# Performance work log

Measured on AMD Instinct MI355X. Metric: run time of the kernel, lower is better.

## Reference

```python
import jax, jax.numpy as jnp
import numpy as np

SCALE_FLOOR = 0.001
N_SOURCES = 16


def setup_inputs() -> dict:
    key = jax.random.key(0)
    ks = jax.random.split(key, 8)
    n, d_in, d = 131072, 1024, 512
    x = jax.random.normal(ks[0], (n, d_in), dtype=jnp.float32)
    source_ids = jax.random.randint(ks[1], (n,), 0, N_SOURCES, dtype=jnp.int64)
    # backbone: single Linear(d_in -> d)
    Wb = jax.random.normal(ks[2], (d_in, d), dtype=jnp.float32) / np.sqrt(d_in)
    bb = jax.random.normal(ks[3], (d,), dtype=jnp.float32) * 0.01
    # pooled head: Linear(d -> 2)
    Wp = jax.random.normal(ks[4], (d, 2), dtype=jnp.float32) / np.sqrt(d)
    bp = jax.random.normal(ks[5], (2,), dtype=jnp.float32) * 0.01
    # per-source heads stacked: [S, d, 2], [S, 2]
    Ws = jax.random.normal(ks[6], (N_SOURCES, d, 2), dtype=jnp.float32) / np.sqrt(d)
    bs = jax.random.normal(ks[7], (N_SOURCES, 2), dtype=jnp.float32) * 0.01
    return {"x": x, "source_ids": source_ids, "Wb": Wb, "bb": bb,
            "Wp": Wp, "bp": bp, "Ws": Ws, "bs": bs}


def _head(raw):
    # raw: (n, 2) -> (mu, scale) with softplus + floor on scale
    mu = raw[:, 0]
    scale = jax.nn.softplus(raw[:, 1]) + SCALE_FLOOR
    return mu, scale


def reference(x, source_ids, Wb, bb, Wp, bp, Ws, bs):
    # backbone embedding: (n, d)
    emb = x @ Wb + bb
    # pooled head
    pooled_mu, pooled_scale = _head(emb @ Wp + bp)
    # routed per-source heads: compute all tiny heads, then gather per row.
    # raw_all: (n, S, 2); S*2 is tiny so this beats gather of per-row weights.
    raw_all = jnp.einsum('nd,sdk->nsk', emb, Ws) + bs[None, :, :]
    raw_sel = jnp.take_along_axis(raw_all, source_ids[:, None, None], axis=1)[:, 0, :]
    src_mu, src_scale = _head(raw_sel)
    # all source ids fall in [0, N_SOURCES), so every row is covered
    # (matches the torch loop where unmatched rows would stay zero).
    return emb, pooled_mu, pooled_scale, src_mu, src_scale
```

## Files before the change

### kernel.cpp

```cpp
#include <hip/hip_runtime.h>

typedef short bf16x8 __attribute__((ext_vector_type(8)));
typedef float f32x4 __attribute__((ext_vector_type(4)));

#define NROWS 131072L
#define DIN 1024
#define DEMB 512
#define NEXT 640

__device__ __forceinline__ unsigned short f2bf(float f) {
  unsigned u = __float_as_uint(f);
  u += 0x7FFFu + ((u >> 16) & 1u);
  return (unsigned short)(u >> 16);
}

__device__ __forceinline__ unsigned pkhi(float a, float b) {
  unsigned ua = __float_as_uint(a) + 0x8000u;
  unsigned ub = __float_as_uint(b) + 0x8000u;
  return __builtin_amdgcn_perm(ub, ua, 0x07060302u);
}

__device__ __forceinline__ float softplusf(float v) {
  return fmaxf(v, 0.f) + log1pf(expf(-fabsf(v)));
}

__global__ __launch_bounds__(256) void wb_transpose(const float* __restrict__ Wb,
                                                    unsigned short* __restrict__ WbT) {
  int g = blockIdx.x * 256 + threadIdx.x;
  int n = g & 511;
  int kb = g >> 9;
  unsigned short tmp[8];
#pragma unroll
  for (int j = 0; j < 8; ++j)
    tmp[j] = f2bf(Wb[(kb * 8 + j) * DEMB + n]);
  uint4 v;
  v.x = (unsigned)tmp[0] | ((unsigned)tmp[1] << 16);
  v.y = (unsigned)tmp[2] | ((unsigned)tmp[3] << 16);
  v.z = (unsigned)tmp[4] | ((unsigned)tmp[5] << 16);
  v.w = (unsigned)tmp[6] | ((unsigned)tmp[7] << 16);
  *(uint4*)(WbT + (long)n * DIN + kb * 8) = v;
}

__global__ void zero_tail(unsigned* __restrict__ p) {
  p[blockIdx.x * 256 + threadIdx.x] = 0u;
}

__global__ __launch_bounds__(256) void wfold_rows(const float* __restrict__ Wb,
                                                  const float* __restrict__ Wp,
                                                  const float* __restrict__ Ws,
                                                  unsigned short* __restrict__ WbT) {
  int w = threadIdx.x >> 6, lane = threadIdx.x & 63;
  int k = blockIdx.x * 4 + w;
  if (lane >= 34) return;
  const float* src;
  if (lane < 2) src = Wp + lane;
  else { int s = (lane - 2) >> 1; src = Ws + s * 1024 + (lane & 1); }
  const float* wrow = Wb + (long)k * DEMB;
  float acc = 0.f;
#pragma unroll 8
  for (int d = 0; d < DEMB; ++d) acc = fmaf(wrow[d], src[2 * d], acc);
  WbT[(long)(512 + lane) * DIN + k] = f2bf(acc);
}

__global__ void bfold_k(const float* __restrict__ bb, const float* __restrict__ Wp,
                        const float* __restrict__ bp, const float* __restrict__ Ws,
                        const float* __restrict__ bs, float* __restrict__ bf) {
  int j = threadIdx.x;
  if (j >= 34) return;
  const float* src; float bias;
  if (j < 2) { src = Wp + j; bias = bp[j]; }
  else { int s = (j - 2) >> 1; src = Ws + s * 1024 + (j & 1); bias = bs[s * 2 + (j & 1)]; }
  float acc = bias;
  for (int d = 0; d < DEMB; ++d) acc = fmaf(bb[d], src[2 * d], acc);
  bf[j] = acc;
}

#define SB __builtin_amdgcn_sched_barrier(0)

__global__ __launch_bounds__(256, 2) void gemm_fused(
    const float* __restrict__ x, const unsigned short* __restrict__ wbt,
    const float* __restrict__ bb, const int* __restrict__ sid,
    const float* __restrict__ bfold, float* __restrict__ out) {
  __shared__ __align__(16) char SM[65536];
  char* const As0 = SM;
  char* const As1 = SM + 16384;
  char* const Bs0 = SM + 32768;
  char* const Bs1 = SM + 49152;

  const int t = threadIdx.x;
  const int lane = t & 63;
  const int wid = t >> 6;
  const int wm = wid >> 1, wn = wid & 1;

  const int bid = blockIdx.x;
  const int swz = (bid & 7) * 640 + (bid >> 3);
  const int mtile = swz / 5;
  const int ntile = swz - mtile * 5;
  const long m0 = (long)mtile * 128;
  const int n0 = ntile * 128;

  const int arow = t >> 4;
  const int acol8 = (t & 15) * 8;
  const int abyte = arow * 128 + (acol8 ^ ((arow & 7) << 4));
  const float* xbase = x + (m0 + arow) * DIN + (t & 15) * 4;

  const int bn = wid * 32 + (lane >> 3);
  const int bg = (lane & 7) ^ (lane >> 3);
  const unsigned short* bsrc = wbt + (long)(n0 + bn) * DIN + bg * 8;

  const int l15 = lane & 15, lg = lane >> 4;
  const int s3 = lane & 7;
  const int kg0 = ((lg ^ s3) << 4);
  const int ardrow = (wm * 64 + l15) * 128;
  const int brdrow = (wn * 64 + l15) * 128;

  f32x4 acc[4][4] = {};
  float4 aA[8], aB[8];

  auto loadA = [&](float4* d, int k0) {
#pragma unroll
    for (int p = 0; p < 8; ++p)
      d[p] = *(const float4*)(xbase + (long)p * 16 * DIN + k0);
  };
  auto stageB = [&](char* Bw, int k0) {
#pragma unroll
    for (int i = 0; i < 4; ++i) {
      const unsigned short* gp = bsrc + (long)i * 8 * DIN + k0;
      __builtin_amdgcn_global_load_lds(
          (const __attribute__((address_space(1))) void*)gp,
          (__attribute__((address_space(3))) void*)(Bw + wid * 4096 + i * 1024),
          16, 0, 0);
    }
  };
  auto writeA = [&](char* Aw, const float4* d) {
#pragma unroll
    for (int p = 0; p < 8; ++p) {
      uint2 v;
      v.x = pkhi(d[p].x, d[p].y);
      v.y = pkhi(d[p].z, d[p].w);
      *(uint2*)(Aw + abyte + p * 2048) = v;
    }
  };
  auto compute = [&](const char* Ac, const char* Bc) {
#pragma unroll
    for (int ks = 0; ks < 2; ++ks) {
      const int kgo = kg0 ^ (ks << 6);
      bf16x8 af[4], bfv[4];
#pragma unroll
      for (int i = 0; i < 4; ++i) {
        af[i]  = *(const bf16x8*)(Ac + ardrow + i * 2048 + kgo);
        bfv[i] = *(const bf16x8*)(Bc + brdrow + i * 2048 + kgo);
      }
      __builtin_amdgcn_s_setprio(1);
#pragma unroll
      for (int mi = 0; mi < 4; ++mi)
#pragma unroll
        for (int ni = 0; ni < 4; ++ni)
          acc[mi][ni] = __builtin_amdgcn_mfma_f32_16x16x32_bf16(af[mi], bfv[ni],
                                                               acc[mi][ni], 0, 0, 0);
      __builtin_amdgcn_s_setprio(0);
    }
  };

  loadA(aA, 0);
  stageB(Bs0, 0);
  SB; asm volatile("s_waitcnt vmcnt(4)" ::: "memory"); SB;
  writeA(As0, aA);
  loadA(aB, 64);
  SB; asm volatile("s_waitcnt vmcnt(8) lgkmcnt(0)" ::: "memory"); SB;
  __builtin_amdgcn_s_barrier();

#pragma unroll 1
  for (int tb = 0; tb < 14; tb += 2) {
    stageB(Bs1, (tb + 1) * 64);
    loadA(aA, (tb + 2) * 64);
    compute(As0, Bs0);
    SB; asm volatile("s_waitcnt vmcnt(12)" ::: "memory"); SB;
    writeA(As1, aB);
    SB; asm volatile("s_waitcnt vmcnt(8) lgkmcnt(0)" ::: "memory"); SB;
    __builtin_amdgcn_s_barrier();
    stageB(Bs0, (tb + 2) * 64);
    loadA(aB, (tb + 3) * 64);
    compute(As1, Bs1);
    SB; asm volatile("s_waitcnt vmcnt(12)" ::: "memory"); SB;
    writeA(As0, aA);
    SB; asm volatile("s_waitcnt vmcnt(8) lgkmcnt(0)" ::: "memory"); SB;
    __builtin_amdgcn_s_barrier();
  }

  stageB(Bs1, 15 * 64);
  compute(As0, Bs0);
  SB; asm volatile("s_waitcnt vmcnt(4)" ::: "memory"); SB;
  writeA(As1, aB);
  SB; asm volatile("s_waitcnt vmcnt(0) lgkmcnt(0)" ::: "memory"); SB;
  __builtin_amdgcn_s_barrier();
  compute(As1, Bs1);

  if (ntile < 4) {
    const int colg = n0 + wn * 64 + l15;
    float bbv[4];
#pragma unroll
    for (int ni = 0; ni < 4; ++ni) bbv[ni] = bb[colg + ni * 16];
#pragma unroll
    for (int mi = 0; mi < 4; ++mi) {
      const long rbase = m0 + wm * 64 + mi * 16 + lg * 4;
#pragma unroll
      for (int ni = 0; ni < 4; ++ni)
#pragma unroll
        for (int r = 0; r < 4; ++r)
          out[(rbase + r) * DEMB + colg + ni * 16] = acc[mi][ni][r] + bbv[ni];
    }
  } else {
    __syncthreads();
    float* hl = (float*)SM;
    if (wn == 0) {
#pragma unroll
      for (int ni = 0; ni < 3; ++ni) {
#pragma unroll
        for (int mi = 0; mi < 4; ++mi)
#pragma unroll
          for (int r = 0; r < 4; ++r) {
            int row = wm * 64 + mi * 16 + lg * 4 + r;
            int col = l15 + ni * 16;
            if (col < 35) hl[row * 35 + col] = acc[mi][ni][r];
          }
      }
    }
    __syncthreads();
    if (t < 128) {
      const long row = m0 + t;
      const int s = sid[row];
      const float v0 = hl[t * 35 + 0] + bfold[0];
      const float v1 = hl[t * 35 + 1] + bfold[1];
      const float v2 = hl[t * 35 + 2 + 2 * s] + bfold[2 + 2 * s];
      const float v3 = hl[t * 35 + 3 + 2 * s] + bfold[3 + 2 * s];
      float* hp = out + NROWS * DEMB;
      hp[row] = v0;
      hp[NROWS + row] = softplusf(v1) + 0.001f;
      hp[2 * NROWS + row] = v2;
      hp[3 * NROWS + row] = softplusf(v3) + 0.001f;
    }
  }
}

extern "C" void kernel_launch(void* const* d_in, const int* in_sizes, int n_in,
                              void* d_out, int out_size, void* d_ws, size_t ws_size,
                              hipStream_t stream) {
  const float* x  = (const float*)d_in[0];
  const int* sid  = (const int*)d_in[1];
  const float* Wb = (const float*)d_in[2];
  const float* bb = (const float*)d_in[3];
  const float* Wp = (const float*)d_in[4];
  const float* bp = (const float*)d_in[5];
  const float* Ws = (const float*)d_in[6];
  const float* bs = (const float*)d_in[7];
  float* out = (float*)d_out;
  unsigned short* WbT = (unsigned short*)d_ws;
  float* bfoldp = (float*)(WbT + (long)NEXT * DIN);

  wb_transpose<<<256, 256, 0, stream>>>(Wb, WbT);
  zero_tail<<<188, 256, 0, stream>>>((unsigned*)(WbT + 546 * DIN));
  wfold_rows<<<256, 256, 0, stream>>>(Wb, Wp, Ws, WbT);
  bfold_k<<<1, 64, 0, stream>>>(bb, Wp, bp, Ws, bs, bfoldp);
  gemm_fused<<<5120, 256, 0, stream>>>(x, WbT, bb, sid, bfoldp, out);
}
```

Measured before the change: 341.7 us.

## Enlarge GEMM tile to 256x256 with 8 waves and interleaved load/MFMA schedule

Changes the fused GEMM from 128x128 tiles with 4 waves to 256x256 tiles with 8 waves per block, using 128KB of LDS and one block per CU. The extended N dimension is padded to 768, so the head columns now occupy a full 256-wide tile. A new per-K-tile schedule interleaves global loads, LDS reads and MFMA groups with barriers. The larger tile raises operand reuse and cuts redundant x reads, but it pads more wasted compute into the head tile, lowers occupancy and adds more barriers.

```diff
diff --git a/kernel.cpp b/kernel.cpp
--- a/kernel.cpp
+++ b/kernel.cpp
@@ -6,7 +6,7 @@
 #define NROWS 131072L
 #define DIN 1024
 #define DEMB 512
-#define NEXT 640
+#define NEXT 768
 
 __device__ __forceinline__ unsigned short f2bf(float f) {
   unsigned u = __float_as_uint(f);
@@ -77,133 +77,162 @@
 
 #define SB __builtin_amdgcn_sched_barrier(0)
 
-__global__ __launch_bounds__(256, 2) void gemm_fused(
+__global__ __launch_bounds__(512, 1) void gemm_fused(
     const float* __restrict__ x, const unsigned short* __restrict__ wbt,
     const float* __restrict__ bb, const int* __restrict__ sid,
     const float* __restrict__ bfold, float* __restrict__ out) {
-  __shared__ __align__(16) char SM[65536];
+  __shared__ __align__(16) char SM[131072];
   char* const As0 = SM;
-  char* const As1 = SM + 16384;
-  char* const Bs0 = SM + 32768;
-  char* const Bs1 = SM + 49152;
+  char* const As1 = SM + 32768;
+  char* const Bs0 = SM + 65536;
+  char* const Bs1 = SM + 98304;
 
   const int t = threadIdx.x;
   const int lane = t & 63;
   const int wid = t >> 6;
-  const int wm = wid >> 1, wn = wid & 1;
+  const int wm = wid >> 2, wn = wid & 3;
 
   const int bid = blockIdx.x;
-  const int swz = (bid & 7) * 640 + (bid >> 3);
-  const int mtile = swz / 5;
-  const int ntile = swz - mtile * 5;
-  const long m0 = (long)mtile * 128;
-  const int n0 = ntile * 128;
+  const int swz = (bid & 7) * 192 + (bid >> 3);
+  const int mtile = swz / 3;
+  const int ntile = swz - mtile * 3;
+  const long m0 = (long)mtile * 256;
+  const int n0 = ntile * 256;
 
   const int arow = t >> 4;
-  const int acol8 = (t & 15) * 8;
-  const int abyte = arow * 128 + (acol8 ^ ((arow & 7) << 4));
+  const int abyte = arow * 128 + (((t & 15) * 8) ^ ((arow & 7) << 4));
   const float* xbase = x + (m0 + arow) * DIN + (t & 15) * 4;
 
-  const int bn = wid * 32 + (lane >> 3);
-  const int bg = (lane & 7) ^ (lane >> 3);
-  const unsigned short* bsrc = wbt + (long)(n0 + bn) * DIN + bg * 8;
+  const int bsg = (t & 7) ^ ((t >> 3) & 7);
+  const unsigned short* bsrc = wbt + (long)(n0 + (t >> 3)) * DIN + bsg * 8;
 
   const int l15 = lane & 15, lg = lane >> 4;
-  const int s3 = lane & 7;
-  const int kg0 = ((lg ^ s3) << 4);
-  const int ardrow = (wm * 64 + l15) * 128;
-  const int brdrow = (wn * 64 + l15) * 128;
-
-  f32x4 acc[4][4] = {};
-  float4 aA[8], aB[8];
-
-  auto loadA = [&](float4* d, int k0) {
-#pragma unroll
-    for (int p = 0; p < 8; ++p)
-      d[p] = *(const float4*)(xbase + (long)p * 16 * DIN + k0);
-  };
-  auto stageB = [&](char* Bw, int k0) {
-#pragma unroll
-    for (int i = 0; i < 4; ++i) {
-      const unsigned short* gp = bsrc + (long)i * 8 * DIN + k0;
+  const int kg0 = ((lg ^ (l15 & 7)) << 4);
+  const int aBase = (wm * 128 + l15) * 128;
+  const int bBase = (wn * 64 + l15) * 128;
+
+  f32x4 acc[8][4] = {};
+  bf16x8 afc[8];
+  float4 areg[8];
+
+  auto loadA4 = [&](int pbase, int k0) {
+#pragma unroll
+    for (int p = 0; p < 4; ++p)
+      areg[pbase + p] = *(const float4*)(xbase + (long)(pbase + p) * 32 * DIN + k0);
+  };
+  auto gloadB2 = [&](char* Bw, int ibase, int k0) {
+#pragma unroll
+    for (int i = 0; i < 2; ++i) {
+      const unsigned short* gp = bsrc + (long)(ibase + i) * 64 * DIN + k0;
       __builtin_amdgcn_global_load_lds(
           (const __attribute__((address_space(1))) void*)gp,
-          (__attribute__((address_space(3))) void*)(Bw + wid * 4096 + i * 1024),
+          (__attribute__((address_space(3))) void*)(Bw + (ibase + i) * 8192 + t * 16),
           16, 0, 0);
     }
   };
-  auto writeA = [&](char* Aw, const float4* d) {
+  auto writeA = [&](char* Aw) {
 #pragma unroll
     for (int p = 0; p < 8; ++p) {
       uint2 v;
-      v.x = pkhi(d[p].x, d[p].y);
-      v.y = pkhi(d[p].z, d[p].w);
-      *(uint2*)(Aw + abyte + p * 2048) = v;
-    }
-  };
-  auto compute = [&](const char* Ac, const char* Bc) {
-#pragma unroll
-    for (int ks = 0; ks < 2; ++ks) {
-      const int kgo = kg0 ^ (ks << 6);
-      bf16x8 af[4], bfv[4];
-#pragma unroll
-      for (int i = 0; i < 4; ++i) {
-        af[i]  = *(const bf16x8*)(Ac + ardrow + i * 2048 + kgo);
-        bfv[i] = *(const bf16x8*)(Bc + brdrow + i * 2048 + kgo);
-      }
-      __builtin_amdgcn_s_setprio(1);
-#pragma unroll
-      for (int mi = 0; mi < 4; ++mi)
-#pragma unroll
-        for (int ni = 0; ni < 4; ++ni)
-          acc[mi][ni] = __builtin_amdgcn_mfma_f32_16x16x32_bf16(af[mi], bfv[ni],
-                                                               acc[mi][ni], 0, 0, 0);
-      __builtin_amdgcn_s_setprio(0);
-    }
-  };
-
-  loadA(aA, 0);
-  stageB(Bs0, 0);
+      v.x = pkhi(areg[p].x, areg[p].y);
+      v.y = pkhi(areg[p].z, areg[p].w);
+      *(uint2*)(Aw + abyte + p * 4096) = v;
+    }
+  };
+  auto readA8 = [&](const char* Ac, int ks) {
+    const int ko = kg0 ^ (ks << 6);
+#pragma unroll
+    for (int mi = 0; mi < 8; ++mi)
+      afc[mi] = *(const bf16x8*)(Ac + aBase + mi * 2048 + ko);
+  };
+  auto mfma16 = [&](bf16x8 b0, bf16x8 b1, int ni) {
+    __builtin_amdgcn_s_setprio(1);
+#pragma unroll
+    for (int mi = 0; mi < 8; ++mi)
+      acc[mi][ni] = __builtin_amdgcn_mfma_f32_16x16x32_bf16(afc[mi], b0, acc[mi][ni], 0, 0, 0);
+#pragma unroll
+    for (int mi = 0; mi < 8; ++mi)
+      acc[mi][ni + 1] = __builtin_amdgcn_mfma_f32_16x16x32_bf16(afc[mi], b1, acc[mi][ni + 1], 0, 0, 0);
+    __builtin_amdgcn_s_setprio(0);
+  };
+  auto bread = [&](const char* Bc, int ni, int ks) {
+    return *(const bf16x8*)(Bc + bBase + ni * 2048 + (kg0 ^ (ks << 6)));
+  };
+
+  auto tileS = [&](const char* Ac, const char* Bc, char* Aw, char* Bw, int kS) {
+    bf16x8 b0, b1;
+    readA8(Ac, 0); b0 = bread(Bc, 0, 0); b1 = bread(Bc, 1, 0);
+    loadA4(0, kS); gloadB2(Bw, 0, kS);
+    __builtin_amdgcn_s_barrier();
+    SB; asm volatile("s_waitcnt lgkmcnt(0)" ::: "memory"); SB;
+    mfma16(b0, b1, 0);
+    __builtin_amdgcn_s_barrier();
+    b0 = bread(Bc, 2, 0); b1 = bread(Bc, 3, 0);
+    loadA4(4, kS); gloadB2(Bw, 2, kS);
+    __builtin_amdgcn_s_barrier();
+    SB; asm volatile("s_waitcnt lgkmcnt(0)" ::: "memory"); SB;
+    mfma16(b0, b1, 2);
+    __builtin_amdgcn_s_barrier();
+    readA8(Ac, 1); b0 = bread(Bc, 0, 1); b1 = bread(Bc, 1, 1);
+    __builtin_amdgcn_s_barrier();
+    SB; asm volatile("s_waitcnt lgkmcnt(0)" ::: "memory"); SB;
+    mfma16(b0, b1, 0);
+    __builtin_amdgcn_s_barrier();
+    b0 = bread(Bc, 2, 1); b1 = bread(Bc, 3, 1);
+    SB; asm volatile("s_waitcnt vmcnt(2)" ::: "memory"); SB;
+    writeA(Aw);
+    __builtin_amdgcn_s_barrier();
+    SB; asm volatile("s_waitcnt lgkmcnt(0)" ::: "memory"); SB;
+    mfma16(b0, b1, 2);
+    SB; asm volatile("s_waitcnt vmcnt(0) lgkmcnt(0)" ::: "memory"); SB;
+    __builtin_amdgcn_s_barrier();
+  };
+  auto tileN = [&](const char* Ac, const char* Bc) {
+    bf16x8 b0, b1;
+    readA8(Ac, 0); b0 = bread(Bc, 0, 0); b1 = bread(Bc, 1, 0);
+    __builtin_amdgcn_s_barrier();
+    SB; asm volatile("s_waitcnt lgkmcnt(0)" ::: "memory"); SB;
+    mfma16(b0, b1, 0);
+    __builtin_amdgcn_s_barrier();
+    b0 = bread(Bc, 2, 0); b1 = bread(Bc, 3, 0);
+    __builtin_amdgcn_s_barrier();
+    SB; asm volatile("s_waitcnt lgkmcnt(0)" ::: "memory"); SB;
+    mfma16(b0, b1, 2);
+    __builtin_amdgcn_s_barrier();
+    readA8(Ac, 1); b0 = bread(Bc, 0, 1); b1 = bread(Bc, 1, 1);
+    __builtin_amdgcn_s_barrier();
+    SB; asm volatile("s_waitcnt lgkmcnt(0)" ::: "memory"); SB;
+    mfma16(b0, b1, 0);
+    __builtin_amdgcn_s_barrier();
+    b0 = bread(Bc, 2, 1); b1 = bread(Bc, 3, 1);
+    __builtin_amdgcn_s_barrier();
+    SB; asm volatile("s_waitcnt lgkmcnt(0)" ::: "memory"); SB;
+    mfma16(b0, b1, 2);
+  };
+
+  loadA4(0, 0); loadA4(4, 0);
+  gloadB2(Bs0, 0, 0); gloadB2(Bs0, 2, 0);
   SB; asm volatile("s_waitcnt vmcnt(4)" ::: "memory"); SB;
-  writeA(As0, aA);
-  loadA(aB, 64);
-  SB; asm volatile("s_waitcnt vmcnt(8) lgkmcnt(0)" ::: "memory"); SB;
+  writeA(As0);
+  SB; asm volatile("s_waitcnt vmcnt(0) lgkmcnt(0)" ::: "memory"); SB;
   __builtin_amdgcn_s_barrier();
 
 #pragma unroll 1
   for (int tb = 0; tb < 14; tb += 2) {
-    stageB(Bs1, (tb + 1) * 64);
-    loadA(aA, (tb + 2) * 64);
-    compute(As0, Bs0);
-    SB; asm volatile("s_waitcnt vmcnt(12)" ::: "memory"); SB;
-    writeA(As1, aB);
-    SB; asm volatile("s_waitcnt vmcnt(8) lgkmcnt(0)" ::: "memory"); SB;
-    __builtin_amdgcn_s_barrier();
-    stageB(Bs0, (tb + 2) * 64);
-    loadA(aB, (tb + 3) * 64);
-    compute(As1, Bs1);
-    SB; asm volatile("s_waitcnt vmcnt(12)" ::: "memory"); SB;
-    writeA(As0, aA);
-    SB; asm volatile("s_waitcnt vmcnt(8) lgkmcnt(0)" ::: "memory"); SB;
-    __builtin_amdgcn_s_barrier();
+    tileS(As0, Bs0, As1, Bs1, (tb + 1) * 64);
+    tileS(As1, Bs1, As0, Bs0, (tb + 2) * 64);
   }
-
-  stageB(Bs1, 15 * 64);
-  compute(As0, Bs0);
-  SB; asm volatile("s_waitcnt vmcnt(4)" ::: "memory"); SB;
-  writeA(As1, aB);
-  SB; asm volatile("s_waitcnt vmcnt(0) lgkmcnt(0)" ::: "memory"); SB;
-  __builtin_amdgcn_s_barrier();
-  compute(As1, Bs1);
-
-  if (ntile < 4) {
+  tileS(As0, Bs0, As1, Bs1, 15 * 64);
+  tileN(As1, Bs1);
+
+  if (ntile < 2) {
     const int colg = n0 + wn * 64 + l15;
     float bbv[4];
 #pragma unroll
     for (int ni = 0; ni < 4; ++ni) bbv[ni] = bb[colg + ni * 16];
 #pragma unroll
-    for (int mi = 0; mi < 4; ++mi) {
-      const long rbase = m0 + wm * 64 + mi * 16 + lg * 4;
+    for (int mi = 0; mi < 8; ++mi) {
+      const long rbase = m0 + wm * 128 + mi * 16 + lg * 4;
 #pragma unroll
       for (int ni = 0; ni < 4; ++ni)
 #pragma unroll
@@ -217,17 +246,17 @@
 #pragma unroll
       for (int ni = 0; ni < 3; ++ni) {
 #pragma unroll
-        for (int mi = 0; mi < 4; ++mi)
+        for (int mi = 0; mi < 8; ++mi)
 #pragma unroll
           for (int r = 0; r < 4; ++r) {
-            int row = wm * 64 + mi * 16 + lg * 4 + r;
-            int col = l15 + ni * 16;
+            int row = wm * 128 + mi * 16 + lg * 4 + r;
+            int col = ni * 16 + l15;
             if (col < 35) hl[row * 35 + col] = acc[mi][ni][r];
           }
       }
     }
     __syncthreads();
-    if (t < 128) {
+    if (t < 256) {
       const long row = m0 + t;
       const int s = sid[row];
       const float v0 = hl[t * 35 + 0] + bfold[0];
@@ -259,8 +288,8 @@
   float* bfoldp = (float*)(WbT + (long)NEXT * DIN);
 
   wb_transpose<<<256, 256, 0, stream>>>(Wb, WbT);
-  zero_tail<<<188, 256, 0, stream>>>((unsigned*)(WbT + 546 * DIN));
+  zero_tail<<<444, 256, 0, stream>>>((unsigned*)(WbT + 546 * DIN));
   wfold_rows<<<256, 256, 0, stream>>>(Wb, Wp, Ws, WbT);
   bfold_k<<<1, 64, 0, stream>>>(bb, Wp, bp, Ws, bs, bfoldp);
-  gemm_fused<<<5120, 256, 0, stream>>>(x, WbT, bb, sid, bfoldp, out);
-}
+  gemm_fused<<<1536, 512, 0, stream>>>(x, WbT, bb, sid, bfoldp, out);
+}
```

After: 359.6 us. +5.2%, slower.

## Triple-buffer B tiles to prefetch two K-steps ahead with one barrier per step

Applied to the files above, without the earlier changes.

Adds a third LDS buffer for the B operand and restructures the main loop so B is staged two K-tiles ahead. Each phase now issues its loads, writes the previous A registers into LDS and computes, using one barrier per K-step instead of two waits per step. The aim is to hide more global-load latency and cut synchronisation stalls. In exchange LDS grows from 64KB to 80KB per block, which may limit how many blocks fit on a CU under launch_bounds(256,2).

```diff
diff --git a/kernel.cpp b/kernel.cpp
--- a/kernel.cpp
+++ b/kernel.cpp
@@ -81,11 +81,12 @@
     const float* __restrict__ x, const unsigned short* __restrict__ wbt,
     const float* __restrict__ bb, const int* __restrict__ sid,
     const float* __restrict__ bfold, float* __restrict__ out) {
-  __shared__ __align__(16) char SM[65536];
+  __shared__ __align__(16) char SM[81920];
   char* const As0 = SM;
   char* const As1 = SM + 16384;
   char* const Bs0 = SM + 32768;
   char* const Bs1 = SM + 49152;
+  char* const Bs2 = SM + 65536;
 
   const int t = threadIdx.x;
   const int lane = t & 63;
@@ -162,39 +163,43 @@
     }
   };
 
+#define PH(BST, ALD, AWS, AWB, AC, BC, TT)                          \
+  stageB(BST, ((TT) + 2) * 64);                                     \
+  loadA(ALD, ((TT) + 2) * 64);                                      \
+  SB; asm volatile("s_waitcnt vmcnt(12)" ::: "memory"); SB;         \
+  writeA(AWS, AWB);                                                 \
+  compute(AC, BC);                                                  \
+  SB; asm volatile("s_waitcnt lgkmcnt(0)" ::: "memory"); SB;        \
+  __builtin_amdgcn_s_barrier();
+
+  stageB(Bs0, 0);
+  stageB(Bs1, 64);
   loadA(aA, 0);
-  stageB(Bs0, 0);
-  SB; asm volatile("s_waitcnt vmcnt(4)" ::: "memory"); SB;
+  loadA(aB, 64);
+  SB; asm volatile("s_waitcnt vmcnt(8)" ::: "memory"); SB;
   writeA(As0, aA);
-  loadA(aB, 64);
-  SB; asm volatile("s_waitcnt vmcnt(8) lgkmcnt(0)" ::: "memory"); SB;
+  SB; asm volatile("s_waitcnt lgkmcnt(0)" ::: "memory"); SB;
   __builtin_amdgcn_s_barrier();
 
 #pragma unroll 1
-  for (int tb = 0; tb < 14; tb += 2) {
-    stageB(Bs1, (tb + 1) * 64);
-    loadA(aA, (tb + 2) * 64);
-    compute(As0, Bs0);
-    SB; asm volatile("s_waitcnt vmcnt(12)" ::: "memory"); SB;
-    writeA(As1, aB);
-    SB; asm volatile("s_waitcnt vmcnt(8) lgkmcnt(0)" ::: "memory"); SB;
-    __builtin_amdgcn_s_barrier();
-    stageB(Bs0, (tb + 2) * 64);
-    loadA(aB, (tb + 3) * 64);
-    compute(As1, Bs1);
-    SB; asm volatile("s_waitcnt vmcnt(12)" ::: "memory"); SB;
-    writeA(As0, aA);
-    SB; asm volatile("s_waitcnt vmcnt(8) lgkmcnt(0)" ::: "memory"); SB;
-    __builtin_amdgcn_s_barrier();
+  for (int tb = 0; tb < 12; tb += 6) {
+    PH(Bs2, aA, As1, aB, As0, Bs0, tb + 0)
+    PH(Bs0, aB, As0, aA, As1, Bs1, tb + 1)
+    PH(Bs1, aA, As1, aB, As0, Bs2, tb + 2)
+    PH(Bs2, aB, As0, aA, As1, Bs0, tb + 3)
+    PH(Bs0, aA, As1, aB, As0, Bs1, tb + 4)
+    PH(Bs1, aB, As0, aA, As1, Bs2, tb + 5)
   }
-
-  stageB(Bs1, 15 * 64);
-  compute(As0, Bs0);
-  SB; asm volatile("s_waitcnt vmcnt(4)" ::: "memory"); SB;
+  PH(Bs2, aA, As1, aB, As0, Bs0, 12)
+  PH(Bs0, aB, As0, aA, As1, Bs1, 13)
+#undef PH
+
+  SB; asm volatile("s_waitcnt vmcnt(0)" ::: "memory"); SB;
   writeA(As1, aB);
-  SB; asm volatile("s_waitcnt vmcnt(0) lgkmcnt(0)" ::: "memory"); SB;
+  compute(As0, Bs2);
+  SB; asm volatile("s_waitcnt lgkmcnt(0)" ::: "memory"); SB;
   __builtin_amdgcn_s_barrier();
-  compute(As1, Bs1);
+  compute(As1, Bs0);
 
   if (ntile < 4) {
     const int colg = n0 + wn * 64 + l15;
```

Result: slower. 370.3 us (+8.4%).

## Enlarge GEMM tile to 512 rows with 8 waves and split-phase A pipeline

Applied to the files above, without the earlier changes.

Increases the block tile from 128x128 to 512x128 using 512 threads (8 waves, each computing 128x64), so each B tile staged in LDS is reused across four times as many rows. This cuts redundant B loads and the per-block prologue/epilogue overhead. The A load/convert/write pipeline is restructured into two half-phases interleaved with the two k-steps, and LDS grows to 160 KB. In exchange, occupancy drops to one block per CU because of LDS size, accumulator register pressure doubles, and latency hiding relies on waves within the block.

```diff
diff --git a/kernel.cpp b/kernel.cpp
--- a/kernel.cpp
+++ b/kernel.cpp
@@ -77,15 +77,15 @@
 
 #define SB __builtin_amdgcn_sched_barrier(0)
 
-__global__ __launch_bounds__(256, 2) void gemm_fused(
+__global__ __launch_bounds__(512, 2) void gemm_fused(
     const float* __restrict__ x, const unsigned short* __restrict__ wbt,
     const float* __restrict__ bb, const int* __restrict__ sid,
     const float* __restrict__ bfold, float* __restrict__ out) {
-  __shared__ __align__(16) char SM[65536];
+  __shared__ __align__(16) char SM[163840];
   char* const As0 = SM;
-  char* const As1 = SM + 16384;
-  char* const Bs0 = SM + 32768;
-  char* const Bs1 = SM + 49152;
+  char* const As1 = SM + 65536;
+  char* const Bs0 = SM + 131072;
+  char* const Bs1 = SM + 147456;
 
   const int t = threadIdx.x;
   const int lane = t & 63;
@@ -93,108 +93,104 @@
   const int wm = wid >> 1, wn = wid & 1;
 
   const int bid = blockIdx.x;
-  const int swz = (bid & 7) * 640 + (bid >> 3);
+  const int swz = (bid & 7) * 160 + (bid >> 3);
   const int mtile = swz / 5;
   const int ntile = swz - mtile * 5;
-  const long m0 = (long)mtile * 128;
+  const long m0 = (long)mtile * 512;
   const int n0 = ntile * 128;
 
   const int arow = t >> 4;
-  const int acol8 = (t & 15) * 8;
-  const int abyte = arow * 128 + (acol8 ^ ((arow & 7) << 4));
+  const int abyte = arow * 128 + (((t & 15) * 8) ^ ((arow & 7) << 4));
   const float* xbase = x + (m0 + arow) * DIN + (t & 15) * 4;
 
-  const int bn = wid * 32 + (lane >> 3);
-  const int bg = (lane & 7) ^ (lane >> 3);
-  const unsigned short* bsrc = wbt + (long)(n0 + bn) * DIN + bg * 8;
+  const int bg = (t & 7) ^ ((t >> 3) & 7);
+  const unsigned short* bsrc = wbt + (long)(n0 + (t >> 3)) * DIN + bg * 8;
+  const int bdst = t * 16;
 
   const int l15 = lane & 15, lg = lane >> 4;
   const int s3 = lane & 7;
   const int kg0 = ((lg ^ s3) << 4);
-  const int ardrow = (wm * 64 + l15) * 128;
+  const int ardrow = (wm * 128 + l15) * 128;
   const int brdrow = (wn * 64 + l15) * 128;
 
-  f32x4 acc[4][4] = {};
-  float4 aA[8], aB[8];
-
-  auto loadA = [&](float4* d, int k0) {
-#pragma unroll
-    for (int p = 0; p < 8; ++p)
-      d[p] = *(const float4*)(xbase + (long)p * 16 * DIN + k0);
+  f32x4 acc[8][4] = {};
+  float4 aR[8];
+
+  auto loadA8 = [&](int k0, int h) {
+#pragma unroll
+    for (int j = 0; j < 8; ++j)
+      aR[j] = *(const float4*)(xbase + (long)(h * 8 + j) * 32 * DIN + k0);
   };
   auto stageB = [&](char* Bw, int k0) {
 #pragma unroll
-    for (int i = 0; i < 4; ++i) {
-      const unsigned short* gp = bsrc + (long)i * 8 * DIN + k0;
+    for (int i = 0; i < 2; ++i) {
+      const unsigned short* gp = bsrc + (long)i * 64 * DIN + k0;
       __builtin_amdgcn_global_load_lds(
           (const __attribute__((address_space(1))) void*)gp,
-          (__attribute__((address_space(3))) void*)(Bw + wid * 4096 + i * 1024),
+          (__attribute__((address_space(3))) void*)(Bw + i * 8192 + bdst),
           16, 0, 0);
     }
   };
-  auto writeA = [&](char* Aw, const float4* d) {
-#pragma unroll
-    for (int p = 0; p < 8; ++p) {
+  auto writeA8 = [&](char* Aw, int h) {
+#pragma unroll
+    for (int j = 0; j < 8; ++j) {
       uint2 v;
-      v.x = pkhi(d[p].x, d[p].y);
-      v.y = pkhi(d[p].z, d[p].w);
-      *(uint2*)(Aw + abyte + p * 2048) = v;
-    }
-  };
-  auto compute = [&](const char* Ac, const char* Bc) {
-#pragma unroll
-    for (int ks = 0; ks < 2; ++ks) {
-      const int kgo = kg0 ^ (ks << 6);
-      bf16x8 af[4], bfv[4];
-#pragma unroll
-      for (int i = 0; i < 4; ++i) {
-        af[i]  = *(const bf16x8*)(Ac + ardrow + i * 2048 + kgo);
-        bfv[i] = *(const bf16x8*)(Bc + brdrow + i * 2048 + kgo);
-      }
-      __builtin_amdgcn_s_setprio(1);
-#pragma unroll
-      for (int mi = 0; mi < 4; ++mi)
-#pragma unroll
-        for (int ni = 0; ni < 4; ++ni)
-          acc[mi][ni] = __builtin_amdgcn_mfma_f32_16x16x32_bf16(af[mi], bfv[ni],
-                                                               acc[mi][ni], 0, 0, 0);
-      __builtin_amdgcn_s_setprio(0);
-    }
-  };
-
-  loadA(aA, 0);
+      v.x = pkhi(aR[j].x, aR[j].y);
+      v.y = pkhi(aR[j].z, aR[j].w);
+      *(uint2*)(Aw + abyte + (h * 8 + j) * 4096) = v;
+    }
+  };
+  auto compute_ks = [&](const char* Ac, const char* Bc, int ks) {
+    const int kgo = kg0 ^ (ks << 6);
+    bf16x8 af[8], bfv[4];
+#pragma unroll
+    for (int i = 0; i < 8; ++i)
+      af[i] = *(const bf16x8*)(Ac + ardrow + i * 2048 + kgo);
+#pragma unroll
+    for (int i = 0; i < 4; ++i)
+      bfv[i] = *(const bf16x8*)(Bc + brdrow + i * 2048 + kgo);
+    __builtin_amdgcn_s_setprio(1);
+#pragma unroll
+    for (int mi = 0; mi < 8; ++mi)
+#pragma unroll
+      for (int ni = 0; ni < 4; ++ni)
+        acc[mi][ni] = __builtin_amdgcn_mfma_f32_16x16x32_bf16(af[mi], bfv[ni],
+                                                             acc[mi][ni], 0, 0, 0);
+    __builtin_amdgcn_s_setprio(0);
+  };
+
+#define PH(AC, BC, AW, BW, TT)                                      \
+  loadA8(((TT) + 1) * 64, 0);                                       \
+  stageB(BW, ((TT) + 1) * 64);                                      \
+  compute_ks(AC, BC, 0);                                            \
+  SB; asm volatile("s_waitcnt vmcnt(2)" ::: "memory"); SB;          \
+  writeA8(AW, 0);                                                   \
+  loadA8(((TT) + 1) * 64, 1);                                       \
+  compute_ks(AC, BC, 1);                                            \
+  SB; asm volatile("s_waitcnt vmcnt(0)" ::: "memory"); SB;          \
+  writeA8(AW, 1);                                                   \
+  SB; asm volatile("s_waitcnt lgkmcnt(0)" ::: "memory"); SB;        \
+  __builtin_amdgcn_s_barrier();
+
+  loadA8(0, 0);
   stageB(Bs0, 0);
-  SB; asm volatile("s_waitcnt vmcnt(4)" ::: "memory"); SB;
-  writeA(As0, aA);
-  loadA(aB, 64);
-  SB; asm volatile("s_waitcnt vmcnt(8) lgkmcnt(0)" ::: "memory"); SB;
+  SB; asm volatile("s_waitcnt vmcnt(2)" ::: "memory"); SB;
+  writeA8(As0, 0);
+  loadA8(0, 1);
+  SB; asm volatile("s_waitcnt vmcnt(2)" ::: "memory"); SB;
+  writeA8(As0, 1);
+  SB; asm volatile("s_waitcnt vmcnt(0) lgkmcnt(0)" ::: "memory"); SB;
   __builtin_amdgcn_s_barrier();
 
 #pragma unroll 1
   for (int tb = 0; tb < 14; tb += 2) {
-    stageB(Bs1, (tb + 1) * 64);
-    loadA(aA, (tb + 2) * 64);
-    compute(As0, Bs0);
-    SB; asm volatile("s_waitcnt vmcnt(12)" ::: "memory"); SB;
-    writeA(As1, aB);
-    SB; asm volatile("s_waitcnt vmcnt(8) lgkmcnt(0)" ::: "memory"); SB;
-    __builtin_amdgcn_s_barrier();
-    stageB(Bs0, (tb + 2) * 64);
-    loadA(aB, (tb + 3) * 64);
-    compute(As1, Bs1);
-    SB; asm volatile("s_waitcnt vmcnt(12)" ::: "memory"); SB;
-    writeA(As0, aA);
-    SB; asm volatile("s_waitcnt vmcnt(8) lgkmcnt(0)" ::: "memory"); SB;
-    __builtin_amdgcn_s_barrier();
+    PH(As0, Bs0, As1, Bs1, tb + 0)
+    PH(As1, Bs1, As0, Bs0, tb + 1)
   }
-
-  stageB(Bs1, 15 * 64);
-  compute(As0, Bs0);
-  SB; asm volatile("s_waitcnt vmcnt(4)" ::: "memory"); SB;
-  writeA(As1, aB);
-  SB; asm volatile("s_waitcnt vmcnt(0) lgkmcnt(0)" ::: "memory"); SB;
-  __builtin_amdgcn_s_barrier();
-  compute(As1, Bs1);
+  PH(As0, Bs0, As1, Bs1, 14)
+#undef PH
+  compute_ks(As1, Bs1, 0);
+  compute_ks(As1, Bs1, 1);
 
   if (ntile < 4) {
     const int colg = n0 + wn * 64 + l15;
@@ -202,8 +198,8 @@
 #pragma unroll
     for (int ni = 0; ni < 4; ++ni) bbv[ni] = bb[colg + ni * 16];
 #pragma unroll
-    for (int mi = 0; mi < 4; ++mi) {
-      const long rbase = m0 + wm * 64 + mi * 16 + lg * 4;
+    for (int mi = 0; mi < 8; ++mi) {
+      const long rbase = m0 + wm * 128 + mi * 16 + lg * 4;
 #pragma unroll
       for (int ni = 0; ni < 4; ++ni)
 #pragma unroll
@@ -217,17 +213,17 @@
 #pragma unroll
       for (int ni = 0; ni < 3; ++ni) {
 #pragma unroll
-        for (int mi = 0; mi < 4; ++mi)
+        for (int mi = 0; mi < 8; ++mi)
 #pragma unroll
           for (int r = 0; r < 4; ++r) {
-            int row = wm * 64 + mi * 16 + lg * 4 + r;
+            int row = wm * 128 + mi * 16 + lg * 4 + r;
             int col = l15 + ni * 16;
             if (col < 35) hl[row * 35 + col] = acc[mi][ni][r];
           }
       }
     }
     __syncthreads();
-    if (t < 128) {
+    {
       const long row = m0 + t;
       const int s = sid[row];
       const float v0 = hl[t * 35 + 0] + bfold[0];
@@ -262,5 +258,5 @@
   zero_tail<<<188, 256, 0, stream>>>((unsigned*)(WbT + 546 * DIN));
   wfold_rows<<<256, 256, 0, stream>>>(Wb, Wp, Ws, WbT);
   bfold_k<<<1, 64, 0, stream>>>(bb, Wp, bp, Ws, bs, bfoldp);
-  gemm_fused<<<5120, 256, 0, stream>>>(x, WbT, bb, sid, bfoldp, out);
-}
+  gemm_fused<<<1280, 512, 0, stream>>>(x, WbT, bb, sid, bfoldp, out);
+}
```

After: 541.2 us. +58.4%, slower.
